# Performance work log

Measured on AMD Instinct MI355X. Metric: run time of the kernel, lower is better.

Reference implementation:

```python
import jax, jax.numpy as jnp
import numpy as np

B, T, D, H = 4, 2048, 1024, 16
DK = D // H
LN_EPS = 1e-5


def setup_inputs() -> dict:
    key = jax.random.key(0)
    ks = jax.random.split(key, 12)
    s = 1.0 / np.sqrt(D)
    inp = {
        'x': jax.random.normal(ks[0], (B, T, D), jnp.float32),
        'Wq': jax.random.normal(ks[1], (D, D), jnp.float32) * s,
        'bq': jnp.zeros((D,), jnp.float32),
        'Wk': jax.random.normal(ks[2], (D, D), jnp.float32) * s,
        'bk': jnp.zeros((D,), jnp.float32),
        'Wv': jax.random.normal(ks[3], (D, D), jnp.float32) * s,
        'bv': jnp.zeros((D,), jnp.float32),
        'Wo': jax.random.normal(ks[4], (D, D), jnp.float32) * s,
        'bo': jnp.zeros((D,), jnp.float32),
        'ln_g': jnp.ones((D,), jnp.float32),
        'ln_b': jnp.zeros((D,), jnp.float32),
    }
    return inp


def reference(x, Wq, bq, Wk, bk, Wv, bv, Wo, bo, ln_g, ln_b):
    b, t, d = x.shape
    scale = jnp.sqrt(jnp.asarray(DK, x.dtype))
    # QKV projections -> [b, h, t, dk]
    q = (x @ Wq + bq).reshape(b, t, H, DK).transpose(0, 2, 1, 3)
    k = (x @ Wk + bk).reshape(b, t, H, DK).transpose(0, 2, 1, 3)
    v = (x @ Wv + bv).reshape(b, t, H, DK).transpose(0, 2, 1, 3)
    scores = jnp.einsum('bhqd,bhkd->bhqk', q, k) / scale  # [b,h,t,t]
    mask = jnp.tril(jnp.ones((t, t), x.dtype))[None, None]  # [1,1,t,t]
    neg = jnp.finfo(x.dtype).min
    scores = jnp.where(mask == 0, neg, scores)
    attn = jax.nn.softmax(scores, axis=-1)
    # mask-renormalize (as in the torch module)
    attn = attn * mask
    denom = attn.sum(-1, keepdims=True)
    attn = jnp.where(denom > 0, attn / denom, jnp.zeros_like(attn))
    ctx = jnp.einsum('bhqk,bhkd->bhqd', attn, v)  # [b,h,t,dk]
    ctx = ctx.transpose(0, 2, 1, 3).reshape(b, t, d)
    out = ctx @ Wo + bo
    y = out + x  # residual
    mu = y.mean(-1, keepdims=True)
    var = ((y - mu) ** 2).mean(-1, keepdims=True)
    return (y - mu) / jnp.sqrt(var + LN_EPS) * ln_g + ln_b
```

## Files before the change

kernel.cpp:

```cpp
#include <hip/hip_runtime.h>


using u16 = unsigned short;
using u32 = unsigned int;
typedef _Float16 f16x8 __attribute__((ext_vector_type(8)));
typedef float f32x4 __attribute__((ext_vector_type(4)));
typedef unsigned short u16x8 __attribute__((ext_vector_type(8)));

template <bool B> struct BoolTag { static constexpr bool v = B; };

__device__ inline u16 f2h_bits(float f) {
    _Float16 h = (_Float16)f;
    return __builtin_bit_cast(u16, h);
}

__device__ __forceinline__ void gload16(const void* g, void* l) {
    __builtin_amdgcn_global_load_lds(
        (const __attribute__((address_space(1))) void*)g,
        (__attribute__((address_space(3))) void*)l, 16, 0, 0);
}

__global__ __launch_bounds__(256) void convert_x_kernel(const float* __restrict__ x,
                                                        u16* __restrict__ xb) {
    size_t i = ((size_t)blockIdx.x * 256 + threadIdx.x) * 8;
    float4 a = *(const float4*)(x + i);
    float4 b = *(const float4*)(x + i + 4);
    u16x8 o;
    o[0] = f2h_bits(a.x); o[1] = f2h_bits(a.y); o[2] = f2h_bits(a.z); o[3] = f2h_bits(a.w);
    o[4] = f2h_bits(b.x); o[5] = f2h_bits(b.y); o[6] = f2h_bits(b.z); o[7] = f2h_bits(b.w);
    *(u16x8*)(xb + i) = o;
}

__global__ __launch_bounds__(256) void convert_wt_kernel(
    const float* __restrict__ W0, const float* __restrict__ W1,
    const float* __restrict__ W2, const float* __restrict__ W3,
    u16* __restrict__ Wt) {
    __shared__ float ts[64][68];
    const int z = blockIdx.z;
    const float* W = z == 0 ? W0 : (z == 1 ? W1 : (z == 2 ? W2 : W3));
    u16* Wo = Wt + (size_t)z * 1048576;
    const int k0 = blockIdx.x * 64, n0 = blockIdx.y * 64;
    const int tid = threadIdx.x, rr = tid >> 3, c = tid & 7;
#pragma unroll
    for (int p = 0; p < 2; p++) {
        int k = p * 32 + rr;
        float4 u = *(const float4*)(W + (size_t)(k0 + k) * 1024 + n0 + c * 8);
        float4 w = *(const float4*)(W + (size_t)(k0 + k) * 1024 + n0 + c * 8 + 4);
        *(float4*)&ts[k][c * 8] = u;
        *(float4*)&ts[k][c * 8 + 4] = w;
    }
    __syncthreads();
#pragma unroll
    for (int p = 0; p < 2; p++) {
        int n = p * 32 + rr;
        u16 o[8];
#pragma unroll
        for (int j = 0; j < 8; j++) o[j] = f2h_bits(ts[c * 8 + j][n]);
        *(u16x8*)(Wo + (size_t)(n0 + n) * 1024 + k0 + c * 8) = *(u16x8*)o;
    }
}

template <int MODE>
__global__ __launch_bounds__(512) void gemm256_kernel(
    const u16* __restrict__ A, const u16* __restrict__ Wt,
    const float* __restrict__ b0, const float* __restrict__ b1,
    const float* __restrict__ b2, u16* __restrict__ qo, u16* __restrict__ ko,
    u16* __restrict__ vt, float* __restrict__ outf,
    const float* __restrict__ xres) {
    constexpr int NBY = (MODE == 0) ? 12 : 4;
    __shared__ u16 As[3][128 * 64];
    __shared__ u16 Bs[3][256 * 64];

    const int bid = blockIdx.x;
    const int cpx = (MODE == 0) ? 96 : 32;
    const int swz = (bid & 7) * cpx + (bid >> 3);
    const int bx = swz / NBY, by = swz % NBY;
    const size_t row0 = (size_t)bx * 128;
    const size_t col0 = (size_t)by * 256;

    const int tid = threadIdx.x, lane = tid & 63;
    const int wid = tid >> 6, wm = wid >> 2, wn = wid & 3;
    const int l15 = lane & 15, lg = lane >> 4;
    const int rr = tid >> 3, c8 = tid & 7;
    const int scw = (c8 ^ (rr & 7)) * 8;

    f32x4 acc[4][4] = {};

    auto stage_half = [&](int kt, u16* dA, u16* dB, int h) {
        const int k0 = kt * 64;
        if (h == 0) {
            gload16(A + (row0 + rr) * 1024 + k0 + scw, dA + tid * 8);
            gload16(Wt + (col0 + rr) * 1024 + k0 + scw, dB + tid * 8);
            gload16(Wt + (col0 + 64 + rr) * 1024 + k0 + scw, dB + (512 + tid) * 8);
        } else {
            gload16(A + (row0 + 64 + rr) * 1024 + k0 + scw, dA + (512 + tid) * 8);
            gload16(Wt + (col0 + 128 + rr) * 1024 + k0 + scw, dB + (1024 + tid) * 8);
            gload16(Wt + (col0 + 192 + rr) * 1024 + k0 + scw, dB + (1536 + tid) * 8);
        }
    };

    auto ldops = [&](const u16* bA, const u16* bB, int kcv, f16x8* Af, f16x8* Bf) {
        const int swo = ((kcv * 4 + lg) ^ (l15 & 7)) * 8;
#pragma unroll
        for (int n = 0; n < 4; n++)
            Bf[n] = *(const f16x8*)(bB + (wn * 64 + n * 16 + l15) * 64 + swo);
#pragma unroll
        for (int m = 0; m < 4; m++)
            Af[m] = *(const f16x8*)(bA + (wm * 64 + m * 16 + l15) * 64 + swo);
    };

    auto domfma = [&](const f16x8* Af, const f16x8* Bf) {
        __builtin_amdgcn_s_setprio(1);
#pragma unroll
        for (int m = 0; m < 4; m++)
#pragma unroll
            for (int n = 0; n < 4; n++)
                acc[m][n] = __builtin_amdgcn_mfma_f32_16x16x32_f16(
                    Af[m], Bf[n], acc[m][n], 0, 0, 0);
        __builtin_amdgcn_s_setprio(0);
    };

    u16 *pA = &As[0][0], *pnA = &As[1][0], *ppA = &As[2][0];
    u16 *pB = &Bs[0][0], *pnB = &Bs[1][0], *ppB = &Bs[2][0];

    stage_half(0, pA, pB, 0);
    stage_half(0, pA, pB, 1);
    stage_half(1, pnA, pnB, 0);
    stage_half(1, pnA, pnB, 1);
    asm volatile("s_waitcnt vmcnt(6)" ::: "memory");
    __builtin_amdgcn_sched_barrier(0);
    __builtin_amdgcn_s_barrier();

#pragma unroll 1
    for (int t = 0; t < 16; t++) {
        f16x8 af[4], bf[4];
        ldops(pA, pB, 0, af, bf);
        if (t < 14) stage_half(t + 2, ppA, ppB, 0);
        __builtin_amdgcn_sched_barrier(0);
        __builtin_amdgcn_s_barrier();
        asm volatile("s_waitcnt lgkmcnt(0)" ::: "memory");
        __builtin_amdgcn_sched_barrier(0);
        domfma(af, bf);
        __builtin_amdgcn_sched_barrier(0);
        __builtin_amdgcn_s_barrier();
        ldops(pA, pB, 1, af, bf);
        if (t < 14) stage_half(t + 2, ppA, ppB, 1);
        if (t < 14)       asm volatile("s_waitcnt vmcnt(6)" ::: "memory");
        else if (t == 14) asm volatile("s_waitcnt vmcnt(0)" ::: "memory");
        __builtin_amdgcn_sched_barrier(0);
        __builtin_amdgcn_s_barrier();
        asm volatile("s_waitcnt lgkmcnt(0)" ::: "memory");
        __builtin_amdgcn_sched_barrier(0);
        domfma(af, bf);
        __builtin_amdgcn_sched_barrier(0);
        if (t < 15) {
            __builtin_amdgcn_s_barrier();
            u16* tp;
            tp = pA; pA = pnA; pnA = ppA; ppA = tp;
            tp = pB; pB = pnB; pnB = ppB; ppB = tp;
        }
    }

    if (MODE == 0) {
        const int zsel = by >> 2;
        if (zsel < 2) {
            u16* ob = zsel == 0 ? qo : ko;
            const float* bias = zsel == 0 ? b0 : b1;
            const float qs = zsel == 0 ? 0.18033688f : 1.0f;
#pragma unroll
            for (int m = 0; m < 4; m++) {
#pragma unroll
                for (int n = 0; n < 4; n++) {
                    size_t col = col0 + wn * 64 + n * 16 + l15;
                    size_t colz = col & 1023;
                    float bb = bias[colz];
#pragma unroll
                    for (int r = 0; r < 4; r++) {
                        size_t row = row0 + wm * 64 + m * 16 + lg * 4 + r;
                        ob[row * 1024 + colz] = f2h_bits((acc[m][n][r] + bb) * qs);
                    }
                }
            }
        } else {
            u16* TL = &Bs[0][0];
            __syncthreads();
#pragma unroll
            for (int m = 0; m < 4; m++) {
#pragma unroll
                for (int n = 0; n < 4; n++) {
                    int cl = wn * 64 + n * 16 + l15;
                    float bb = b2[(col0 & 1023) + cl];
#pragma unroll
                    for (int r = 0; r < 4; r++) {
                        int rl = wm * 64 + m * 16 + lg * 4 + r;
                        TL[cl * 136 + rl] = f2h_bits(acc[m][n][r] + bb);
                    }
                }
            }
            __syncthreads();
            const int vrl = tid >> 1, th = tid & 1;
            size_t vrow = (row0 >> 11) * 1024 + (col0 & 1023) + vrl;
            const int t0loc = (int)(row0 & 2047) + th * 64;
#pragma unroll
            for (int j = 0; j < 8; j++)
                *(u16x8*)(vt + vrow * 2048 + t0loc + j * 8) =
                    *(const u16x8*)(TL + vrl * 136 + th * 64 + j * 8);
        }
    } else {
#pragma unroll
        for (int m = 0; m < 4; m++) {
#pragma unroll
            for (int n = 0; n < 4; n++) {
                size_t col = col0 + wn * 64 + n * 16 + l15;
                float bb = b0[col];
#pragma unroll
                for (int r = 0; r < 4; r++) {
                    size_t row = row0 + wm * 64 + m * 16 + lg * 4 + r;
                    size_t idx = row * 1024 + col;
                    outf[idx] = acc[m][n][r] + bb + xres[idx];
                }
            }
        }
    }
}

__global__ __launch_bounds__(512) void attn_kernel(const u16* __restrict__ Q,
                                                   const u16* __restrict__ Kb,
                                                   const u16* __restrict__ Vt,
                                                   u16* __restrict__ ctx) {
    __shared__ u16 Ks[2][64 * 64];
    __shared__ u16 Vs[2][64 * 64];
    __shared__ u16 Ps[8][2][16][72];

    const int bh = blockIdx.x;
    const int b = bh >> 4, h = bh & 15;
    const int qb = 7 - (int)blockIdx.y;
    const int tid = threadIdx.x, lane = tid & 63, wid = tid >> 6;
    const int l15 = lane & 15, lg = lane >> 4;
    const int q0w = qb * 256 + wid * 32;
    const int send = qb * 256;

    const int rr = tid >> 3, c8 = tid & 7;
    const int scw = (c8 ^ (rr & 7)) * 8;
    const size_t kbase = ((size_t)b * 2048) * 1024 + h * 64 + scw;
    const size_t vbase = ((size_t)bh * 64 + rr) * 2048 + scw;

    f16x8 qv[2][2];
#pragma unroll
    for (int qf = 0; qf < 2; qf++) {
        size_t qoff = ((size_t)b * 2048 + q0w + qf * 16 + l15) * 1024 + h * 64 + lg * 8;
        qv[qf][0] = *(const f16x8*)(Q + qoff);
        qv[qf][1] = *(const f16x8*)(Q + qoff + 32);
    }

    const int swk0 = (lg ^ (l15 & 7)) * 8;
    const int swk1 = ((4 + lg) ^ (l15 & 7)) * 8;
    u16* Pw0 = &Ps[wid][0][0][0] + l15 * 72;
    u16* Pw1 = &Ps[wid][1][0][0] + l15 * 72;

    f32x4 acc[2][4] = {};
    float psum[2] = {0.0f, 0.0f};

    auto stage = [&](int s, int bf) {
        gload16(Kb + kbase + (size_t)(s + rr) * 1024, Ks[bf] + tid * 8);
        gload16(Vt + vbase + s, Vs[bf] + tid * 8);
    };

    auto body = [&](int s, int bf, auto maskc) {
        constexpr bool MASK = decltype(maskc)::v;
        f32x4 sc[2][4];
#pragma unroll
        for (int c = 0; c < 4; c++) {
            const u16* kp = Ks[bf] + (c * 16 + l15) * 64;
            f16x8 kf0 = *(const f16x8*)(kp + swk0);
            f16x8 kf1 = *(const f16x8*)(kp + swk1);
#pragma unroll
            for (int qf = 0; qf < 2; qf++) {
                f32x4 z = {};
                z = __builtin_amdgcn_mfma_f32_16x16x32_f16(kf0, qv[qf][0], z, 0, 0, 0);
                z = __builtin_amdgcn_mfma_f32_16x16x32_f16(kf1, qv[qf][1], z, 0, 0, 0);
                sc[qf][c] = z;
            }
        }
#pragma unroll
        for (int qf = 0; qf < 2; qf++) {
            u16* Pw = qf ? Pw1 : Pw0;
#pragma unroll
            for (int c = 0; c < 4; c++) {
                float pv[4];
#pragma unroll
                for (int r = 0; r < 4; r++) {
                    float e = __builtin_amdgcn_exp2f(fminf(sc[qf][c][r], 15.0f));
                    if (MASK) {
                        int kk = s + c * 16 + lg * 4 + r;
                        e = (kk <= q0w + qf * 16 + l15) ? e : 0.0f;
                    }
                    psum[qf] += e;
                    pv[r] = e;
                }
                uint2 w;
                w.x = __builtin_bit_cast(u32, __builtin_amdgcn_cvt_pkrtz(pv[0], pv[1]));
                w.y = __builtin_bit_cast(u32, __builtin_amdgcn_cvt_pkrtz(pv[2], pv[3]));
                *(uint2*)(Pw + c * 16 + lg * 4) = w;
            }
        }
        f16x8 pa0[2], pa1[2];
#pragma unroll
        for (int qf = 0; qf < 2; qf++) {
            const u16* Pw = qf ? Pw1 : Pw0;
            pa0[qf] = *(const f16x8*)(Pw + lg * 8);
            pa1[qf] = *(const f16x8*)(Pw + 32 + lg * 8);
        }
#pragma unroll
        for (int dt = 0; dt < 4; dt++) {
            const u16* vp = Vs[bf] + (dt * 16 + l15) * 64;
            f16x8 vf0 = *(const f16x8*)(vp + swk0);
            f16x8 vf1 = *(const f16x8*)(vp + swk1);
#pragma unroll
            for (int qf = 0; qf < 2; qf++) {
                acc[qf][dt] =
                    __builtin_amdgcn_mfma_f32_16x16x32_f16(pa0[qf], vf0, acc[qf][dt], 0, 0, 0);
                acc[qf][dt] =
                    __builtin_amdgcn_mfma_f32_16x16x32_f16(pa1[qf], vf1, acc[qf][dt], 0, 0, 0);
            }
        }
    };

    stage(0, 0);
    int cur = 0;
    for (int s = 0; s < send; s += 64) {
        __syncthreads();
        stage(s + 64, cur ^ 1);
        body(s, cur, BoolTag<false>{});
        cur ^= 1;
    }
#pragma unroll 1
    for (int j = 0; j < 4; j++) {
        __syncthreads();
        if (j < 3) stage(send + 64 * (j + 1), cur ^ 1);
        if (wid >= 2 * j) body(send + 64 * j, cur, BoolTag<true>{});
        cur ^= 1;
    }

#pragma unroll
    for (int qf = 0; qf < 2; qf++) {
        psum[qf] += __shfl_xor(psum[qf], 16);
        psum[qf] += __shfl_xor(psum[qf], 32);
    }
#pragma unroll
    for (int qf = 0; qf < 2; qf++) {
        float inv = 1.0f / psum[qf];
#pragma unroll
        for (int r = 0; r < 4; r++) {
            float ir = __shfl(inv, lg * 4 + r);
            size_t row = (size_t)b * 2048 + q0w + qf * 16 + lg * 4 + r;
#pragma unroll
            for (int dt = 0; dt < 4; dt++)
                ctx[row * 1024 + h * 64 + dt * 16 + l15] = f2h_bits(acc[qf][dt][r] * ir);
        }
    }
}

__global__ __launch_bounds__(256) void ln_kernel(const float* __restrict__ y,
                                                 const float* __restrict__ g,
                                                 const float* __restrict__ bb,
                                                 float* __restrict__ out) {
    const int r = blockIdx.x, tid = threadIdx.x;
    float4 v = *(const float4*)(y + (size_t)r * 1024 + tid * 4);
    float s = v.x + v.y + v.z + v.w;
    float sq = v.x * v.x + v.y * v.y + v.z * v.z + v.w * v.w;
#pragma unroll
    for (int ofs = 1; ofs < 64; ofs <<= 1) {
        s += __shfl_xor(s, ofs);
        sq += __shfl_xor(sq, ofs);
    }
    __shared__ float as[4], aq[4];
    if ((tid & 63) == 0) { as[tid >> 6] = s; aq[tid >> 6] = sq; }
    __syncthreads();
    s = as[0] + as[1] + as[2] + as[3];
    sq = aq[0] + aq[1] + aq[2] + aq[3];
    float mu = s * (1.0f / 1024.0f);
    float var = sq * (1.0f / 1024.0f) - mu * mu;
    float rstd = rsqrtf(var + 1e-5f);
    float4 gv = *(const float4*)(g + tid * 4);
    float4 bv = *(const float4*)(bb + tid * 4);
    float4 o4;
    o4.x = (v.x - mu) * rstd * gv.x + bv.x;
    o4.y = (v.y - mu) * rstd * gv.y + bv.y;
    o4.z = (v.z - mu) * rstd * gv.z + bv.z;
    o4.w = (v.w - mu) * rstd * gv.w + bv.w;
    *(float4*)(out + (size_t)r * 1024 + tid * 4) = o4;
}

extern "C" void kernel_launch(void* const* d_in, const int* in_sizes, int n_in,
                              void* d_out, int out_size, void* d_ws, size_t ws_size,
                              hipStream_t stream) {
    const float* x  = (const float*)d_in[0];
    const float* Wq = (const float*)d_in[1];
    const float* bq = (const float*)d_in[2];
    const float* Wk = (const float*)d_in[3];
    const float* bk = (const float*)d_in[4];
    const float* Wv = (const float*)d_in[5];
    const float* bv = (const float*)d_in[6];
    const float* Wo = (const float*)d_in[7];
    const float* bo = (const float*)d_in[8];
    const float* lg = (const float*)d_in[9];
    const float* lb = (const float*)d_in[10];
    float* out = (float*)d_out;

    char* ws = (char*)d_ws;
    u16* xb = (u16*)(ws + 0);
    u16* wt = (u16*)(ws + 16777216);
    u16* q  = (u16*)(ws + 25165824);
    u16* k  = (u16*)(ws + 41943040);
    u16* vt = (u16*)(ws + 75497472);
    u16* cx = (u16*)(ws + 92274688);
    float* y = (float*)(ws + 109051904);

    convert_x_kernel<<<4096, 256, 0, stream>>>(x, xb);
    convert_wt_kernel<<<dim3(16, 16, 4), 256, 0, stream>>>(Wq, Wk, Wv, Wo, wt);

    gemm256_kernel<0><<<768, 512, 0, stream>>>(xb, wt, bq, bk, bv, q, k, vt,
                                               nullptr, nullptr);
    attn_kernel<<<dim3(64, 8), 512, 0, stream>>>(q, k, vt, cx);
    gemm256_kernel<1><<<256, 512, 0, stream>>>(cx, wt + 3145728, bo, nullptr,
                                               nullptr, nullptr, nullptr, nullptr,
                                               y, x);
    ln_kernel<<<8192, 256, 0, stream>>>(y, lg, lb, out);
}
```

Baseline: 189.2 us.

## Use 256x256 tiles with double-buffered LDS for the QKV projection GEMM

Splits the templated GEMM into a dedicated QKV kernel and a Wo kernel. The QKV kernel grows the tile from 128x256 to 256x256, so 384 blocks run instead of 768. Each block keeps 8x4 MFMA accumulators per wave and double-buffers 64-wide K slices in 128KB of LDS, with finer-grained phases that interleave loads and MFMAs. This is meant to raise arithmetic intensity and cut redundant global loads of A and W, at the cost of more registers, lower occupancy, full vmcnt(0) waits, and a two-pass epilogue for the transposed V store.

Result: no change. 188.4 us (-0.4%).

```diff
diff --git a/kernel.cpp b/kernel.cpp
--- a/kernel.cpp
+++ b/kernel.cpp
@@ -19,6 +19,15 @@
         (const __attribute__((address_space(1))) void*)g,
         (__attribute__((address_space(3))) void*)l, 16, 0, 0);
 }
+
+#define PH_SYNC()                                            \
+    __builtin_amdgcn_sched_barrier(0);                       \
+    __builtin_amdgcn_s_barrier();                            \
+    asm volatile("s_waitcnt lgkmcnt(0)" ::: "memory");       \
+    __builtin_amdgcn_sched_barrier(0)
+#define PH_END()                                             \
+    __builtin_amdgcn_sched_barrier(0);                       \
+    __builtin_amdgcn_s_barrier()
 
 __global__ __launch_bounds__(256) void convert_x_kernel(const float* __restrict__ x,
                                                         u16* __restrict__ xb) {
@@ -60,21 +69,163 @@
     }
 }
 
-template <int MODE>
-__global__ __launch_bounds__(512) void gemm256_kernel(
+__global__ __launch_bounds__(512) void gemm_qkv256_kernel(
     const u16* __restrict__ A, const u16* __restrict__ Wt,
-    const float* __restrict__ b0, const float* __restrict__ b1,
-    const float* __restrict__ b2, u16* __restrict__ qo, u16* __restrict__ ko,
-    u16* __restrict__ vt, float* __restrict__ outf,
+    const float* __restrict__ bq, const float* __restrict__ bk,
+    const float* __restrict__ bv, u16* __restrict__ qo, u16* __restrict__ ko,
+    u16* __restrict__ vt) {
+    __shared__ u16 SH[65536];
+    u16* const Ab0 = SH;
+    u16* const Ab1 = SH + 16384;
+    u16* const Bb0 = SH + 32768;
+    u16* const Bb1 = SH + 49152;
+
+    const int bid = blockIdx.x;
+    const int swz = (bid & 7) * 48 + (bid >> 3);
+    const int bx = swz / 12, by = swz % 12;
+    const size_t row0 = (size_t)bx * 256;
+    const size_t col0 = (size_t)by * 256;
+
+    const int tid = threadIdx.x, lane = tid & 63;
+    const int wid = tid >> 6, wm = wid >> 2, wn = wid & 3;
+    const int l15 = lane & 15, lg = lane >> 4;
+    const int rr = tid >> 3, c8 = tid & 7;
+    const int scw = (c8 ^ (rr & 7)) * 8;
+
+    f32x4 acc[8][4] = {};
+    f16x8 af[4], bf[4];
+
+    auto stageA = [&](int kt, u16* dst) {
+#pragma unroll
+        for (int g = 0; g < 4; g++)
+            gload16(A + (row0 + g * 64 + rr) * 1024 + kt * 64 + scw,
+                    dst + (g * 512 + tid) * 8);
+    };
+    auto stageB = [&](int kt, u16* dst) {
+#pragma unroll
+        for (int g = 0; g < 4; g++)
+            gload16(Wt + (col0 + g * 64 + rr) * 1024 + kt * 64 + scw,
+                    dst + (g * 512 + tid) * 8);
+    };
+    auto ldB4 = [&](const u16* Bb, int kc) {
+#pragma unroll
+        for (int n = 0; n < 4; n++) {
+            int rb = wn * 64 + n * 16 + l15;
+            bf[n] = *(const f16x8*)(Bb + rb * 64 + ((kc * 4 + lg) ^ (rb & 7)) * 8);
+        }
+    };
+    auto ldA4 = [&](const u16* Abf, int kc, int half) {
+#pragma unroll
+        for (int m = 0; m < 4; m++) {
+            int ra = wm * 128 + half * 64 + m * 16 + l15;
+            af[m] = *(const f16x8*)(Abf + ra * 64 + ((kc * 4 + lg) ^ (ra & 7)) * 8);
+        }
+    };
+    auto mf16 = [&](int half) {
+        __builtin_amdgcn_s_setprio(1);
+#pragma unroll
+        for (int m = 0; m < 4; m++)
+#pragma unroll
+            for (int n = 0; n < 4; n++)
+                acc[half * 4 + m][n] = __builtin_amdgcn_mfma_f32_16x16x32_f16(
+                    af[m], bf[n], acc[half * 4 + m][n], 0, 0, 0);
+        __builtin_amdgcn_s_setprio(0);
+    };
+
+    stageA(0, Ab0); stageB(0, Bb0);
+    stageA(1, Ab1); stageB(1, Bb1);
+    asm volatile("s_waitcnt vmcnt(8)" ::: "memory");
+    __builtin_amdgcn_sched_barrier(0);
+    __builtin_amdgcn_s_barrier();
+
+#pragma unroll 1
+    for (int t = 0; t < 8; t++) {
+        ldB4(Bb0, 0); ldA4(Ab0, 0, 0);
+        if (t >= 1) stageA(2 * t + 1, Ab1);
+        PH_SYNC(); mf16(0); PH_END();
+        ldA4(Ab0, 0, 1);
+        if (t >= 1) stageB(2 * t + 1, Bb1);
+        PH_SYNC(); mf16(1); PH_END();
+        ldB4(Bb0, 1); ldA4(Ab0, 1, 0);
+        PH_SYNC(); mf16(0); PH_END();
+        ldA4(Ab0, 1, 1);
+        asm volatile("s_waitcnt vmcnt(0)" ::: "memory");
+        PH_SYNC(); mf16(1); PH_END();
+        ldB4(Bb1, 0); ldA4(Ab1, 0, 0);
+        if (t < 7) stageA(2 * t + 2, Ab0);
+        PH_SYNC(); mf16(0); PH_END();
+        ldA4(Ab1, 0, 1);
+        if (t < 7) stageB(2 * t + 2, Bb0);
+        PH_SYNC(); mf16(1); PH_END();
+        ldB4(Bb1, 1); ldA4(Ab1, 1, 0);
+        PH_SYNC(); mf16(0); PH_END();
+        ldA4(Ab1, 1, 1);
+        asm volatile("s_waitcnt vmcnt(0)" ::: "memory");
+        PH_SYNC(); mf16(1); PH_END();
+    }
+
+    const int zsel = by >> 2;
+    if (zsel < 2) {
+        u16* ob = zsel == 0 ? qo : ko;
+        const float* bias = zsel == 0 ? bq : bk;
+        const float qs = zsel == 0 ? 0.18033688f : 1.0f;
+#pragma unroll
+        for (int m = 0; m < 8; m++) {
+#pragma unroll
+            for (int n = 0; n < 4; n++) {
+                size_t col = col0 + wn * 64 + n * 16 + l15;
+                size_t colz = col & 1023;
+                float bb = bias[colz];
+#pragma unroll
+                for (int r = 0; r < 4; r++) {
+                    size_t row = row0 + wm * 128 + m * 16 + lg * 4 + r;
+                    ob[row * 1024 + colz] = f2h_bits((acc[m][n][r] + bb) * qs);
+                }
+            }
+        }
+    } else {
+        const int dz0 = (by - 8) * 256;
+        const int b = bx >> 3;
+        const int tloc = (bx & 7) * 256;
+        const int vcl = tid >> 1, th = tid & 1;
+#pragma unroll 1
+        for (int h = 0; h < 2; h++) {
+            __syncthreads();
+            if (wm == h) {
+#pragma unroll
+                for (int m = 0; m < 8; m++) {
+#pragma unroll
+                    for (int n = 0; n < 4; n++) {
+                        int cl = wn * 64 + n * 16 + l15;
+                        float bb = bv[dz0 + cl];
+#pragma unroll
+                        for (int r = 0; r < 4; r++) {
+                            int rl = m * 16 + lg * 4 + r;
+                            SH[cl * 136 + rl] = f2h_bits(acc[m][n][r] + bb);
+                        }
+                    }
+                }
+            }
+            __syncthreads();
+            size_t vrow = (size_t)b * 1024 + dz0 + vcl;
+#pragma unroll
+            for (int j = 0; j < 8; j++)
+                *(u16x8*)(vt + vrow * 2048 + tloc + h * 128 + th * 64 + j * 8) =
+                    *(const u16x8*)(SH + vcl * 136 + th * 64 + j * 8);
+        }
+    }
+}
+
+__global__ __launch_bounds__(512) void gemm_wo_kernel(
+    const u16* __restrict__ A, const u16* __restrict__ Wt,
+    const float* __restrict__ b0, float* __restrict__ outf,
     const float* __restrict__ xres) {
-    constexpr int NBY = (MODE == 0) ? 12 : 4;
     __shared__ u16 As[3][128 * 64];
     __shared__ u16 Bs[3][256 * 64];
 
     const int bid = blockIdx.x;
-    const int cpx = (MODE == 0) ? 96 : 32;
-    const int swz = (bid & 7) * cpx + (bid >> 3);
-    const int bx = swz / NBY, by = swz % NBY;
+    const int swz = (bid & 7) * 32 + (bid >> 3);
+    const int bx = swz / 4, by = swz % 4;
     const size_t row0 = (size_t)bx * 128;
     const size_t col0 = (size_t)by * 256;
 
@@ -136,22 +287,12 @@
         f16x8 af[4], bf[4];
         ldops(pA, pB, 0, af, bf);
         if (t < 14) stage_half(t + 2, ppA, ppB, 0);
-        __builtin_amdgcn_sched_barrier(0);
-        __builtin_amdgcn_s_barrier();
-        asm volatile("s_waitcnt lgkmcnt(0)" ::: "memory");
-        __builtin_amdgcn_sched_barrier(0);
-        domfma(af, bf);
-        __builtin_amdgcn_sched_barrier(0);
-        __builtin_amdgcn_s_barrier();
+        PH_SYNC(); domfma(af, bf); PH_END();
         ldops(pA, pB, 1, af, bf);
         if (t < 14) stage_half(t + 2, ppA, ppB, 1);
         if (t < 14)       asm volatile("s_waitcnt vmcnt(6)" ::: "memory");
         else if (t == 14) asm volatile("s_waitcnt vmcnt(0)" ::: "memory");
-        __builtin_amdgcn_sched_barrier(0);
-        __builtin_amdgcn_s_barrier();
-        asm volatile("s_waitcnt lgkmcnt(0)" ::: "memory");
-        __builtin_amdgcn_sched_barrier(0);
-        domfma(af, bf);
+        PH_SYNC(); domfma(af, bf);
         __builtin_amdgcn_sched_barrier(0);
         if (t < 15) {
             __builtin_amdgcn_s_barrier();
@@ -161,64 +302,17 @@
         }
     }
 
-    if (MODE == 0) {
-        const int zsel = by >> 2;
-        if (zsel < 2) {
-            u16* ob = zsel == 0 ? qo : ko;
-            const float* bias = zsel == 0 ? b0 : b1;
-            const float qs = zsel == 0 ? 0.18033688f : 1.0f;
-#pragma unroll
-            for (int m = 0; m < 4; m++) {
-#pragma unroll
-                for (int n = 0; n < 4; n++) {
-                    size_t col = col0 + wn * 64 + n * 16 + l15;
-                    size_t colz = col & 1023;
-                    float bb = bias[colz];
-#pragma unroll
-                    for (int r = 0; r < 4; r++) {
-                        size_t row = row0 + wm * 64 + m * 16 + lg * 4 + r;
-                        ob[row * 1024 + colz] = f2h_bits((acc[m][n][r] + bb) * qs);
-                    }
-                }
-            }
-        } else {
-            u16* TL = &Bs[0][0];
-            __syncthreads();
-#pragma unroll
-            for (int m = 0; m < 4; m++) {
-#pragma unroll
-                for (int n = 0; n < 4; n++) {
-                    int cl = wn * 64 + n * 16 + l15;
-                    float bb = b2[(col0 & 1023) + cl];
-#pragma unroll
-                    for (int r = 0; r < 4; r++) {
-                        int rl = wm * 64 + m * 16 + lg * 4 + r;
-                        TL[cl * 136 + rl] = f2h_bits(acc[m][n][r] + bb);
-                    }
-                }
-            }
-            __syncthreads();
-            const int vrl = tid >> 1, th = tid & 1;
-            size_t vrow = (row0 >> 11) * 1024 + (col0 & 1023) + vrl;
-            const int t0loc = (int)(row0 & 2047) + th * 64;
-#pragma unroll
-            for (int j = 0; j < 8; j++)
-                *(u16x8*)(vt + vrow * 2048 + t0loc + j * 8) =
-                    *(const u16x8*)(TL + vrl * 136 + th * 64 + j * 8);
-        }
-    } else {
-#pragma unroll
-        for (int m = 0; m < 4; m++) {
-#pragma unroll
-            for (int n = 0; n < 4; n++) {
-                size_t col = col0 + wn * 64 + n * 16 + l15;
-                float bb = b0[col];
-#pragma unroll
-                for (int r = 0; r < 4; r++) {
-                    size_t row = row0 + wm * 64 + m * 16 + lg * 4 + r;
-                    size_t idx = row * 1024 + col;
-                    outf[idx] = acc[m][n][r] + bb + xres[idx];
-                }
+#pragma unroll
+    for (int m = 0; m < 4; m++) {
+#pragma unroll
+        for (int n = 0; n < 4; n++) {
+            size_t col = col0 + wn * 64 + n * 16 + l15;
+            float bb = b0[col];
+#pragma unroll
+            for (int r = 0; r < 4; r++) {
+                size_t row = row0 + wm * 64 + m * 16 + lg * 4 + r;
+                size_t idx = row * 1024 + col;
+                outf[idx] = acc[m][n][r] + bb + xres[idx];
             }
         }
     }
@@ -420,11 +514,8 @@
     convert_x_kernel<<<4096, 256, 0, stream>>>(x, xb);
     convert_wt_kernel<<<dim3(16, 16, 4), 256, 0, stream>>>(Wq, Wk, Wv, Wo, wt);
 
-    gemm256_kernel<0><<<768, 512, 0, stream>>>(xb, wt, bq, bk, bv, q, k, vt,
-                                               nullptr, nullptr);
+    gemm_qkv256_kernel<<<384, 512, 0, stream>>>(xb, wt, bq, bk, bv, q, k, vt);
     attn_kernel<<<dim3(64, 8), 512, 0, stream>>>(q, k, vt, cx);
-    gemm256_kernel<1><<<256, 512, 0, stream>>>(cx, wt + 3145728, bo, nullptr,
-                                               nullptr, nullptr, nullptr, nullptr,
-                                               y, x);
+    gemm_wo_kernel<<<256, 512, 0, stream>>>(cx, wt + 3145728, bo, y, x);
     ln_kernel<<<8192, 256, 0, stream>>>(y, lg, lb, out);
 }
```
